# Optimization experiments

Hardware: AMD Instinct MI355X
Metric: run time of the kernel (lower is better)

The kernel has to match this reference:

```python
import jax, jax.numpy as jnp
import numpy as np

# Four fixed 3x3 directional Laplacian kernels, stacked as OIHW [4,1,3,3]
_KERNELS = jnp.asarray(np.array([
    [[0, 0, 0], [1, -2, 1], [0, 0, 0]],
    [[0, 1, 0], [0, -2, 0], [0, 1, 0]],
    [[0, 0, 1], [0, -2, 0], [1, 0, 0]],
    [[1, 0, 0], [0, -2, 0], [0, 0, 1]],
], dtype=np.float32))[:, None, :, :]


def setup_inputs() -> dict:
    key = jax.random.key(0)
    x = jax.random.normal(key, (16, 3, 512, 512), dtype=jnp.float32)
    return {"x": x}


def reference(x):
    B, C, H, W = x.shape  # C == 3
    # Treat each channel as an independent single-channel image: [B*C, 1, H, W]
    xc = x.reshape(B * C, 1, H, W)
    # One conv producing all 4 directional Laplacians at once: [B*C, 4, H, W]
    lap = jax.lax.conv_general_dilated(
        xc, _KERNELS.astype(x.dtype),
        window_strides=(1, 1), padding=((1, 1), (1, 1)),
        dimension_numbers=("NCHW", "OIHW", "NCHW"))
    # Max over the 4 directions, restore [B, C, H, W]
    out = lap.max(axis=1).reshape(B, C, H, W)
    return out
```

## Files before the change

kernel.cpp:

```cpp
#include <hip/hip_runtime.h>


#define HH 512
#define WW 512
#define IMG (HH * WW)

struct Row {
    float c[4];
    float l, r;
};

__device__ __forceinline__ float getv(const Row& rw, int j) {
    if (j < 0) return rw.l;
    if (j > 3) return rw.r;
    return rw.c[j];
}

__global__ __launch_bounds__(256) void lapmax_kernel(const float* __restrict__ x,
                                                     float* __restrict__ out) {
    const int tid = blockIdx.x * 256 + threadIdx.x;
    const int wq  = tid & 127;
    const int rg  = (tid >> 7) & 127;
    const int img = tid >> 14;

    const int w  = wq << 2;
    const int h0 = rg << 2;

    const float* base  = x   + (size_t)img * IMG;
    float*       obase = out + (size_t)img * IMG;

    Row rows[3];

#pragma unroll
    for (int k = 0; k < 6; ++k) {
        const int r = h0 - 1 + k;
        Row& rw = rows[k % 3];
        if (r >= 0 && r < HH) {
            const float* p = base + r * WW + w;
            const float4 v = *reinterpret_cast<const float4*>(p);
            rw.c[0] = v.x; rw.c[1] = v.y; rw.c[2] = v.z; rw.c[3] = v.w;
            rw.l = (w > 0)       ? p[-1] : 0.0f;
            rw.r = (w < WW - 4)  ? p[4]  : 0.0f;
        } else {
            rw.c[0] = rw.c[1] = rw.c[2] = rw.c[3] = 0.0f;
            rw.l = 0.0f; rw.r = 0.0f;
        }

        if (k >= 2) {
            const Row& up  = rows[(k - 2) % 3];
            const Row& mid = rows[(k - 1) % 3];
            const Row& dn  = rows[k % 3];
            float o[4];
#pragma unroll
            for (int j = 0; j < 4; ++j) {
                const float sh  = getv(mid, j - 1) + getv(mid, j + 1);
                const float sv  = getv(up,  j)     + getv(dn,  j);
                const float sd1 = getv(up,  j + 1) + getv(dn,  j - 1);
                const float sd2 = getv(up,  j - 1) + getv(dn,  j + 1);
                const float m = fmaxf(fmaxf(sh, sv), fmaxf(sd1, sd2));
                o[j] = fmaf(-2.0f, mid.c[j], m);
            }
            const int orow = h0 + k - 2;
            *reinterpret_cast<float4*>(obase + (size_t)orow * WW + w) =
                make_float4(o[0], o[1], o[2], o[3]);
        }
    }
}

extern "C" void kernel_launch(void* const* d_in, const int* in_sizes, int n_in,
                              void* d_out, int out_size, void* d_ws, size_t ws_size,
                              hipStream_t stream) {
    const float* x = (const float*)d_in[0];
    float* out = (float*)d_out;

    const int total    = in_sizes[0];
    const int nthreads = total / 16;
    const int blocks   = (nthreads + 255) / 256;

    lapmax_kernel<<<blocks, 256, 0, stream>>>(x, out);
}
```

Measured before the change: 100.9 us.

## Use wave-per-row-strip tiling with lane shuffles for halos and XCD-aware block mapping

Each 64-lane wave now owns a full 512-wide row strip of 8 rows, with every lane holding 8 columns. Left and right halo values come from neighbour lanes via shuffles instead of extra scalar global loads. Blocks are remapped so contiguous work lands on the same XCD, which should improve L2 locality. Vertical halo overhead drops from 6 loads per 4 rows to 10 per 8 rows, in exchange for more registers per thread and fewer threads overall.

New measurement: 102.1 us. Within noise of the previous version (+1.2%).

```diff
diff --git a/kernel.cpp b/kernel.cpp
--- a/kernel.cpp
+++ b/kernel.cpp
@@ -4,45 +4,61 @@
 #define HH 512
 #define WW 512
 #define IMG (HH * WW)
+#define RS 8
+#define STRIPS (HH / RS)
+
+typedef float f32x4 __attribute__((ext_vector_type(4)));
 
 struct Row {
-    float c[4];
+    float c[8];
     float l, r;
 };
 
 __device__ __forceinline__ float getv(const Row& rw, int j) {
     if (j < 0) return rw.l;
-    if (j > 3) return rw.r;
+    if (j > 7) return rw.r;
     return rw.c[j];
 }
 
 __global__ __launch_bounds__(256) void lapmax_kernel(const float* __restrict__ x,
-                                                     float* __restrict__ out) {
-    const int tid = blockIdx.x * 256 + threadIdx.x;
-    const int wq  = tid & 127;
-    const int rg  = (tid >> 7) & 127;
-    const int img = tid >> 14;
+                                                     float* __restrict__ out,
+                                                     int ntasks) {
+    const int nblk = gridDim.x;
+    const int q = nblk >> 3, rr = nblk & 7;
+    const int xcd = blockIdx.x & 7, idx = blockIdx.x >> 3;
+    const int lb = (xcd < rr ? xcd * (q + 1) : rr * (q + 1) + (xcd - rr) * q) + idx;
 
-    const int w  = wq << 2;
-    const int h0 = rg << 2;
+    const int lane = threadIdx.x & 63;
+    const int task = (lb << 2) + (threadIdx.x >> 6);
+    if (task >= ntasks) return;
 
-    const float* base  = x   + (size_t)img * IMG;
-    float*       obase = out + (size_t)img * IMG;
+    const int img   = task / STRIPS;
+    const int strip = task % STRIPS;
+    const int h0  = strip * RS;
+    const int col = lane << 3;
+
+    const float* __restrict__ base  = x   + (size_t)img * IMG + col;
+    float* __restrict__       obase = out + (size_t)img * IMG + col;
 
     Row rows[3];
 
 #pragma unroll
-    for (int k = 0; k < 6; ++k) {
+    for (int k = 0; k < RS + 2; ++k) {
         const int r = h0 - 1 + k;
         Row& rw = rows[k % 3];
         if (r >= 0 && r < HH) {
-            const float* p = base + r * WW + w;
-            const float4 v = *reinterpret_cast<const float4*>(p);
-            rw.c[0] = v.x; rw.c[1] = v.y; rw.c[2] = v.z; rw.c[3] = v.w;
-            rw.l = (w > 0)       ? p[-1] : 0.0f;
-            rw.r = (w < WW - 4)  ? p[4]  : 0.0f;
+            const float* p = base + (size_t)r * WW;
+            const f32x4 a = *reinterpret_cast<const f32x4*>(p);
+            const f32x4 b = *reinterpret_cast<const f32x4*>(p + 4);
+            rw.c[0] = a[0]; rw.c[1] = a[1]; rw.c[2] = a[2]; rw.c[3] = a[3];
+            rw.c[4] = b[0]; rw.c[5] = b[1]; rw.c[6] = b[2]; rw.c[7] = b[3];
+            const float lv = __shfl_up(rw.c[7], 1);
+            const float rv = __shfl_down(rw.c[0], 1);
+            rw.l = (lane == 0)  ? 0.0f : lv;
+            rw.r = (lane == 63) ? 0.0f : rv;
         } else {
-            rw.c[0] = rw.c[1] = rw.c[2] = rw.c[3] = 0.0f;
+#pragma unroll
+            for (int j = 0; j < 8; ++j) rw.c[j] = 0.0f;
             rw.l = 0.0f; rw.r = 0.0f;
         }
 
@@ -50,19 +66,19 @@
             const Row& up  = rows[(k - 2) % 3];
             const Row& mid = rows[(k - 1) % 3];
             const Row& dn  = rows[k % 3];
-            float o[4];
+            float o[8];
 #pragma unroll
-            for (int j = 0; j < 4; ++j) {
+            for (int j = 0; j < 8; ++j) {
                 const float sh  = getv(mid, j - 1) + getv(mid, j + 1);
-                const float sv  = getv(up,  j)     + getv(dn,  j);
-                const float sd1 = getv(up,  j + 1) + getv(dn,  j - 1);
-                const float sd2 = getv(up,  j - 1) + getv(dn,  j + 1);
+                const float sv  = up.c[j] + dn.c[j];
+                const float sd1 = getv(up, j + 1) + getv(dn, j - 1);
+                const float sd2 = getv(up, j - 1) + getv(dn, j + 1);
                 const float m = fmaxf(fmaxf(sh, sv), fmaxf(sd1, sd2));
                 o[j] = fmaf(-2.0f, mid.c[j], m);
             }
-            const int orow = h0 + k - 2;
-            *reinterpret_cast<float4*>(obase + (size_t)orow * WW + w) =
-                make_float4(o[0], o[1], o[2], o[3]);
+            float* po = obase + (size_t)(h0 + k - 2) * WW;
+            *reinterpret_cast<f32x4*>(po)     = f32x4{ o[0], o[1], o[2], o[3] };
+            *reinterpret_cast<f32x4*>(po + 4) = f32x4{ o[4], o[5], o[6], o[7] };
         }
     }
 }
@@ -73,9 +89,10 @@
     const float* x = (const float*)d_in[0];
     float* out = (float*)d_out;
 
-    const int total    = in_sizes[0];
-    const int nthreads = total / 16;
-    const int blocks   = (nthreads + 255) / 256;
+    const int total  = in_sizes[0];
+    const int nimg   = total / IMG;
+    const int ntasks = nimg * STRIPS;
+    const int blocks = (ntasks + 3) / 4;
 
-    lapmax_kernel<<<blocks, 256, 0, stream>>>(x, out);
+    lapmax_kernel<<<blocks, 256, 0, stream>>>(x, out, ntasks);
 }
```
